# Performance work log

Hardware: AMD Instinct MI355X
Metric: run time of the kernel (lower is better)

The kernel has to match this reference:

```python
import jax, jax.numpy as jnp
import numpy as np

EMBEDDING_DIM = 256
NUM_EMBEDDINGS = 2048
COMMITMENT_COST = 0.25


def setup_inputs() -> dict:
    key = jax.random.key(0)
    k1, k2 = jax.random.split(key)
    inputs = jax.random.normal(k1, (32, EMBEDDING_DIM, 32, 32), dtype=jnp.float32)
    # learned codebook buffer, shape (D, K) as in the torch module
    embedding = jax.random.normal(k2, (EMBEDDING_DIM, NUM_EMBEDDINGS), dtype=jnp.float32)
    return {"inputs": inputs, "embedding": embedding}


def reference(inputs, embedding):
    # Eval-mode forward of VectorQuantizerEMA (EMA buffer updates are
    # training-only side effects and do not affect the returned values).
    B, D, H, W = inputs.shape
    K = embedding.shape[1]
    x = inputs.astype(jnp.float32)
    # (B, D, H, W) -> (N, D), N = B*H*W, clamped as in the source
    flat = jnp.clip(jnp.transpose(x, (0, 2, 3, 1)).reshape(-1, D), -10.0, 10.0)
    # squared L2 distances to every codeword: (N, K)
    distances = (
        jnp.sum(flat * flat, axis=1, keepdims=True)
        + jnp.sum(embedding * embedding, axis=0, keepdims=True)
        - 2.0 * (flat @ embedding)
    )
    encoding_indices = jnp.argmin(distances, axis=1)  # (N,)
    # one-hot @ emb.T is just a gather of codebook columns
    q_flat = jnp.take(embedding.T, encoding_indices, axis=0)  # (N, D)
    quantized = jnp.transpose(q_flat.reshape(B, H, W, D), (0, 3, 1, 2))
    # VQ losses (computed against the un-clamped float inputs, as in torch)
    e_latent_loss = jnp.mean((jax.lax.stop_gradient(quantized) - x) ** 2)
    q_latent_loss = jnp.mean((quantized - jax.lax.stop_gradient(x)) ** 2)
    loss = q_latent_loss + COMMITMENT_COST * e_latent_loss
    # straight-through estimator
    quantized_st = inputs + jax.lax.stop_gradient(quantized - inputs)
    # perplexity from codeword usage (mean one-hot == normalized counts)
    n = encoding_indices.shape[0]
    avg_probs = jnp.zeros((K,), dtype=jnp.float32).at[encoding_indices].add(1.0) / n
    perplexity = jnp.exp(-jnp.sum(avg_probs * jnp.log(avg_probs + 1e-10)))
    return quantized_st, loss, perplexity, encoding_indices
```

## Files before the change

kernel.cpp:

```cpp
#include <hip/hip_runtime.h>
#include <hip/hip_bf16.h>
#include <math.h>

typedef unsigned int  uint;
typedef unsigned short ushort;

#define DD    256
#define KK    2048
#define HW    1024
#define NN    32768
#define NUMEL 8388608
#define STRIDEB (DD*HW)

#define WS_H2     0
#define WS_COUNTS 8192
#define WS_EBF    16512
#define WS_PV     2113664
#define WS_PI     2375808

#define OUT_LOSS  8388608
#define OUT_PPL   8388609
#define OUT_IDX   8388610

typedef __attribute__((ext_vector_type(8))) short  short8;
typedef __attribute__((ext_vector_type(4))) float  float4v;

typedef __attribute__((address_space(1))) uint guint;
typedef __attribute__((address_space(3))) uint luint;

__device__ __forceinline__ ushort f2bf(float f) {
    uint u = __float_as_uint(f);
    return (ushort)((u + 0x7FFFu + ((u >> 16) & 1u)) >> 16);
}

__global__ __launch_bounds__(256) void prep_emb(const float* __restrict__ emb,
                                                ushort* __restrict__ ebf,
                                                float* __restrict__ h2) {
    int g  = blockIdx.x * 256 + threadIdx.x;
    int k  = g & (KK - 1);
    int dg = g >> 11;
    int d0 = dg * 8;
    int s    = dg >> 2;
    int quad = dg & 3;
    int ct   = k >> 4;
    int l    = quad * 16 + (k & 15);

    union { ushort us[8]; uint4 v; } hu, lu;
    float p2 = 0.f;
#pragma unroll
    for (int j = 0; j < 8; ++j) {
        float v = emb[(size_t)(d0 + j) * KK + k];
        p2 += v * v;
        ushort hb = f2bf(v);
        float  hf = __uint_as_float(((uint)hb) << 16);
        hu.us[j] = hb;
        lu.us[j] = f2bf(v - hf);
    }
    size_t hi_off = (size_t)(((ct * 8 + s) * 2 + 0) * 64 + l) * 8;
    size_t lo_off = (size_t)(((ct * 8 + s) * 2 + 1) * 64 + l) * 8;
    *(uint4*)(ebf + hi_off) = hu.v;
    *(uint4*)(ebf + lo_off) = lu.v;
    atomicAdd(&h2[k], 0.5f * p2);
}

__global__ __launch_bounds__(256, 2) void argmin_mfma(
    const float*  __restrict__ x,
    const ushort* __restrict__ ebf,
    const float*  __restrict__ h2,
    float* __restrict__ pv,
    int*   __restrict__ pi)
{
    __shared__ ushort sB[2][8192];
    __shared__ float  sH2[1024];

    const int tid  = threadIdx.x;
    const int w    = tid >> 6;
    const int lane = tid & 63;
    const int m    = lane & 15;
    const int quad = lane >> 4;

    const int rb = blockIdx.x >> 1;
    const int ch = blockIdx.x & 1;
    const int n0 = rb * 128 + w * 32;
    const int b  = n0 >> 10;
    const int hwb = n0 & 1023;
    const float* xb = x + (size_t)b * STRIDEB;
    const int cbase = ch * 1024;
    const int ctg0  = cbase >> 4;

    auto stage = [&](ushort* dst, int ctg) {
        const char* gs = (const char*)(ebf + (size_t)ctg * 8192) + tid * 16;
        char*       ls = (char*)dst + tid * 16;
#pragma unroll
        for (int i = 0; i < 4; ++i)
            __builtin_amdgcn_global_load_lds((guint*)(gs + i * 4096),
                                             (luint*)(ls + i * 4096),
                                             16, 0, 0);
    };

    stage(sB[0], ctg0);
    ((float4*)sH2)[tid] = ((const float4*)(h2 + cbase))[tid];

    short8 xh[2][8], xl[2][8];
    float xs2[2] = {0.f, 0.f};
#pragma unroll
    for (int st = 0; st < 2; ++st) {
        const int hw = hwb + st * 16 + m;
#pragma unroll
        for (int s = 0; s < 8; ++s) {
            const float* p = xb + (size_t)(s * 32 + quad * 8) * HW + hw;
            short8 hh, ll;
#pragma unroll
            for (int j = 0; j < 8; ++j) {
                float v = p[(size_t)j * HW];
                v = fminf(fmaxf(v, -10.f), 10.f);
                xs2[st] += v * v;
                ushort hb = f2bf(v);
                float  hf = __uint_as_float(((uint)hb) << 16);
                hh[j] = (short)hb;
                ll[j] = (short)f2bf(v - hf);
            }
            xh[st][s] = hh;
            xl[st][s] = ll;
        }
    }
#pragma unroll
    for (int st = 0; st < 2; ++st) {
        xs2[st] += __shfl_xor(xs2[st], 16, 64);
        xs2[st] += __shfl_xor(xs2[st], 32, 64);
    }

    float bv[2][4] = {{1e30f,1e30f,1e30f,1e30f},{1e30f,1e30f,1e30f,1e30f}};
    int   bi[2][4] = {{0,0,0,0},{0,0,0,0}};

    auto compute_tile = [&](const ushort* sbc, int ct) {
        float4v ahh0 = {0,0,0,0}, ahl0 = {0,0,0,0}, alh0 = {0,0,0,0};
        float4v ahh1 = {0,0,0,0}, ahl1 = {0,0,0,0}, alh1 = {0,0,0,0};
#pragma unroll
        for (int s = 0; s < 8; ++s) {
            short8 eh = *(const short8*)&sbc[(s * 2 + 0) * 512 + lane * 8];
            short8 el = *(const short8*)&sbc[(s * 2 + 1) * 512 + lane * 8];
            alh0 = __builtin_amdgcn_mfma_f32_16x16x32_bf16(xl[0][s], eh, alh0, 0, 0, 0);
            ahl0 = __builtin_amdgcn_mfma_f32_16x16x32_bf16(xh[0][s], el, ahl0, 0, 0, 0);
            ahh0 = __builtin_amdgcn_mfma_f32_16x16x32_bf16(xh[0][s], eh, ahh0, 0, 0, 0);
            alh1 = __builtin_amdgcn_mfma_f32_16x16x32_bf16(xl[1][s], eh, alh1, 0, 0, 0);
            ahl1 = __builtin_amdgcn_mfma_f32_16x16x32_bf16(xh[1][s], el, ahl1, 0, 0, 0);
            ahh1 = __builtin_amdgcn_mfma_f32_16x16x32_bf16(xh[1][s], eh, ahh1, 0, 0, 0);
        }
        const int c  = cbase + ct * 16 + m;
        const float hv = sH2[ct * 16 + m];
#pragma unroll
        for (int i = 0; i < 4; ++i) {
            float s0 = hv - (ahh0[i] + (ahl0[i] + alh0[i]));
            float s1 = hv - (ahh1[i] + (ahl1[i] + alh1[i]));
            if (s0 < bv[0][i]) { bv[0][i] = s0; bi[0][i] = c; }
            if (s1 < bv[1][i]) { bv[1][i] = s1; bi[1][i] = c; }
        }
    };

    __syncthreads();

    for (int ct = 0; ct < 64; ct += 2) {
        stage(sB[1], ctg0 + ct + 1);
        compute_tile(sB[0], ct);
        __syncthreads();
        stage(sB[0], (ct + 2 < 64) ? (ctg0 + ct + 2) : ctg0);
        compute_tile(sB[1], ct + 1);
        __syncthreads();
    }

#pragma unroll
    for (int st = 0; st < 2; ++st) {
#pragma unroll
        for (int i = 0; i < 4; ++i) {
            float v  = bv[st][i];
            int   ix = bi[st][i];
#pragma unroll
            for (int msk = 8; msk >= 1; msk >>= 1) {
                float ov = __shfl_xor(v, msk, 64);
                int   oi = __shfl_xor(ix, msk, 64);
                if (ov < v || (ov == v && oi < ix)) { v = ov; ix = oi; }
            }
            float xr = __shfl(xs2[st], quad * 4 + i, 16);
            if (m == 0) {
                int n = n0 + st * 16 + quad * 4 + i;
                pv[n * 2 + ch] = xr + 2.0f * v;
                pi[n * 2 + ch] = ix;
            }
        }
    }
}

__global__ __launch_bounds__(256) void quant_kernel(
    const float* __restrict__ emb,
    const float* __restrict__ pv,
    const int*   __restrict__ pi,
    float* __restrict__ out_idx_f,
    int*   __restrict__ counts,
    float* __restrict__ outq)
{
    __shared__ float sE[4096];
    __shared__ int   sIdx[1024];

    const int tid  = threadIdx.x;
    const int bidx = blockIdx.x;
    const int b    = bidx >> 7;
    const int dp   = bidx & 127;
    const int d0   = dp * 2;
    const int nbase = b * HW;

    {
        const float4* src = (const float4*)(emb + (size_t)d0 * KK);
        float4* dst = (float4*)sE;
#pragma unroll
        for (int i = 0; i < 4; ++i) dst[tid + i * 256] = src[tid + i * 256];
    }
    {
        const int n = nbase + tid * 4;
        const float4* pv4 = (const float4*)(pv + (size_t)n * 2);
        const int4*   pi4 = (const int4*)(pi + (size_t)n * 2);
        float4 pva = pv4[0], pvb = pv4[1];
        int4   pia = pi4[0], pib = pi4[1];
        int i0 = (pva.y < pva.x) ? pia.y : pia.x;
        int i1 = (pva.w < pva.z) ? pia.w : pia.z;
        int i2 = (pvb.y < pvb.x) ? pib.y : pib.x;
        int i3 = (pvb.w < pvb.z) ? pib.w : pib.z;
        i0 = min(max(i0, 0), KK - 1); i1 = min(max(i1, 0), KK - 1);
        i2 = min(max(i2, 0), KK - 1); i3 = min(max(i3, 0), KK - 1);
        sIdx[tid * 4 + 0] = i0; sIdx[tid * 4 + 1] = i1;
        sIdx[tid * 4 + 2] = i2; sIdx[tid * 4 + 3] = i3;
        if (d0 == 0) {
            float4 ixf = { (float)i0, (float)i1, (float)i2, (float)i3 };
            *(float4*)(out_idx_f + n) = ixf;
            atomicAdd(&counts[i0], 1);
            atomicAdd(&counts[i1], 1);
            atomicAdd(&counts[i2], 1);
            atomicAdd(&counts[i3], 1);
        }
    }
    __syncthreads();

    {
        const int e   = tid * 8;
        const int dl  = e >> 10;
        const int hw0 = e & 1023;
        const float* row = sE + dl * 2048;
        float q[8];
#pragma unroll
        for (int j = 0; j < 8; ++j) q[j] = row[sIdx[hw0 + j]];
        float4 q0 = { q[0], q[1], q[2], q[3] };
        float4 q1 = { q[4], q[5], q[6], q[7] };
        float* dst = outq + (size_t)bidx * 2048 + e;
        *(float4*)(dst + 0) = q0;
        *(float4*)(dst + 4) = q1;
    }
}

__global__ __launch_bounds__(1024) void finalize_kernel(
    const int* __restrict__ counts,
    const float* __restrict__ pv,
    float* __restrict__ out)
{
    __shared__ float redp[16], redl[16];
    int tid = threadIdx.x;
    float s = 0.f;
#pragma unroll
    for (int k = tid; k < KK; k += 1024) {
        float p = (float)counts[k] * (1.0f / (float)NN);
        s += p * logf(p + 1e-10f);
    }
    float ls = 0.f;
    for (int n = tid; n < NN; n += 1024) {
        float2 pp = *(const float2*)(pv + (size_t)n * 2);
        ls += fminf(pp.x, pp.y);
    }
#pragma unroll
    for (int off = 32; off > 0; off >>= 1) {
        s  += __shfl_down(s, off, 64);
        ls += __shfl_down(ls, off, 64);
    }
    if ((tid & 63) == 0) { redp[tid >> 6] = s; redl[tid >> 6] = ls; }
    __syncthreads();
    if (tid == 0) {
        float tot = 0.f, lsum = 0.f;
#pragma unroll
        for (int i = 0; i < 16; ++i) { tot += redp[i]; lsum += redl[i]; }
        out[OUT_PPL]  = expf(-tot);
        out[OUT_LOSS] = lsum * 1.25f / (float)NUMEL;
    }
}

extern "C" void kernel_launch(void* const* d_in, const int* in_sizes, int n_in,
                              void* d_out, int out_size, void* d_ws, size_t ws_size,
                              hipStream_t stream) {
    const float* x   = (const float*)d_in[0];
    const float* emb = (const float*)d_in[1];
    float* out = (float*)d_out;
    char*  ws  = (char*)d_ws;

    float*  h2     = (float*)(ws + WS_H2);
    int*    counts = (int*)(ws + WS_COUNTS);
    ushort* ebf    = (ushort*)(ws + WS_EBF);
    float*  pv     = (float*)(ws + WS_PV);
    int*    pi     = (int*)(ws + WS_PI);

    hipMemsetAsync(ws, 0, 16384, stream);
    prep_emb<<<256, 256, 0, stream>>>(emb, ebf, h2);
    argmin_mfma<<<512, 256, 0, stream>>>(x, ebf, h2, pv, pi);
    quant_kernel<<<4096, 256, 0, stream>>>(emb, pv, pi,
                                           out + OUT_IDX, counts, out);
    finalize_kernel<<<1, 1024, 0, stream>>>(counts, pv, out);
}
```

Before: 209.0 us.

## Fuse finalize into quant kernel, drop memset and atomics, compute loss directly

Removes the memset and the finalize kernel launch. Counts and the done flag are now zeroed in prep_emb, and the final perplexity and loss reduction runs in the last quant block, found via an atomic done counter. Per-codeword norm partials are written without atomics and summed in argmin, and the x-norm computation is dropped from argmin. Loss is instead recomputed from quant output minus x, which costs an extra read of x in quant_kernel. Indices are stored as ushort. Together these cut launch and sync overhead, at the cost of extra traffic and a last-block serialized reduction.

```diff
diff --git a/kernel.cpp b/kernel.cpp
--- a/kernel.cpp
+++ b/kernel.cpp
@@ -11,18 +11,22 @@
 #define NN    32768
 #define NUMEL 8388608
 #define STRIDEB (DD*HW)
-
-#define WS_H2     0
-#define WS_COUNTS 8192
-#define WS_EBF    16512
-#define WS_PV     2113664
-#define WS_PI     2375808
+#define NQBLK 4096
+
+#define WS_H2P    0
+#define WS_COUNTS 131072
+#define WS_DONE   139264
+#define WS_EBF    139392
+#define WS_PV     2236544
+#define WS_PI     2498688
+#define WS_BPART  WS_H2P
 
 #define OUT_LOSS  8388608
 #define OUT_PPL   8388609
 #define OUT_IDX   8388610
 
 typedef __attribute__((ext_vector_type(8))) short  short8;
+typedef __attribute__((ext_vector_type(8))) ushort ushort8;
 typedef __attribute__((ext_vector_type(4))) float  float4v;
 
 typedef __attribute__((address_space(1))) uint guint;
@@ -35,40 +39,49 @@
 
 __global__ __launch_bounds__(256) void prep_emb(const float* __restrict__ emb,
                                                 ushort* __restrict__ ebf,
-                                                float* __restrict__ h2) {
-    int g  = blockIdx.x * 256 + threadIdx.x;
-    int k  = g & (KK - 1);
-    int dg = g >> 11;
-    int d0 = dg * 8;
-    int s    = dg >> 2;
-    int quad = dg & 3;
-    int ct   = k >> 4;
-    int l    = quad * 16 + (k & 15);
-
-    union { ushort us[8]; uint4 v; } hu, lu;
+                                                float* __restrict__ h2p,
+                                                int* __restrict__ counts,
+                                                int* __restrict__ done) {
+    int g   = blockIdx.x * 256 + threadIdx.x;
+    int k   = g & (KK - 1);
+    int dg2 = g >> 11;
+    int ct  = k >> 4;
     float p2 = 0.f;
 #pragma unroll
-    for (int j = 0; j < 8; ++j) {
-        float v = emb[(size_t)(d0 + j) * KK + k];
-        p2 += v * v;
-        ushort hb = f2bf(v);
-        float  hf = __uint_as_float(((uint)hb) << 16);
-        hu.us[j] = hb;
-        lu.us[j] = f2bf(v - hf);
-    }
-    size_t hi_off = (size_t)(((ct * 8 + s) * 2 + 0) * 64 + l) * 8;
-    size_t lo_off = (size_t)(((ct * 8 + s) * 2 + 1) * 64 + l) * 8;
-    *(uint4*)(ebf + hi_off) = hu.v;
-    *(uint4*)(ebf + lo_off) = lu.v;
-    atomicAdd(&h2[k], 0.5f * p2);
+    for (int h = 0; h < 2; ++h) {
+        int dg = dg2 * 2 + h;
+        int d0 = dg * 8;
+        int s    = dg >> 2;
+        int quad = dg & 3;
+        int l    = quad * 16 + (k & 15);
+        union { ushort us[8]; uint4 v; } hu, lu;
+#pragma unroll
+        for (int j = 0; j < 8; ++j) {
+            float v = emb[(size_t)(d0 + j) * KK + k];
+            p2 += v * v;
+            ushort hb = f2bf(v);
+            float  hf = __uint_as_float(((uint)hb) << 16);
+            hu.us[j] = hb;
+            lu.us[j] = f2bf(v - hf);
+        }
+        size_t hi_off = (size_t)(((ct * 8 + s) * 2 + 0) * 64 + l) * 8;
+        size_t lo_off = (size_t)(((ct * 8 + s) * 2 + 1) * 64 + l) * 8;
+        *(uint4*)(ebf + hi_off) = hu.v;
+        *(uint4*)(ebf + lo_off) = lu.v;
+    }
+    h2p[dg2 * 2048 + k] = 0.5f * p2;
+    if (blockIdx.x == 0) {
+        for (int i = threadIdx.x; i < KK; i += 256) counts[i] = 0;
+        if (threadIdx.x == 0) *done = 0;
+    }
 }
 
 __global__ __launch_bounds__(256, 2) void argmin_mfma(
     const float*  __restrict__ x,
     const ushort* __restrict__ ebf,
-    const float*  __restrict__ h2,
-    float* __restrict__ pv,
-    int*   __restrict__ pi)
+    const float*  __restrict__ h2p,
+    float*  __restrict__ pv,
+    ushort* __restrict__ pi)
 {
     __shared__ ushort sB[2][8192];
     __shared__ float  sH2[1024];
@@ -99,10 +112,17 @@
     };
 
     stage(sB[0], ctg0);
-    ((float4*)sH2)[tid] = ((const float4*)(h2 + cbase))[tid];
+    {
+        float4 a = {0.f, 0.f, 0.f, 0.f};
+#pragma unroll
+        for (int d = 0; d < 16; ++d) {
+            float4 v = ((const float4*)(h2p + d * 2048 + cbase))[tid];
+            a.x += v.x; a.y += v.y; a.z += v.z; a.w += v.w;
+        }
+        ((float4*)sH2)[tid] = a;
+    }
 
     short8 xh[2][8], xl[2][8];
-    float xs2[2] = {0.f, 0.f};
 #pragma unroll
     for (int st = 0; st < 2; ++st) {
         const int hw = hwb + st * 16 + m;
@@ -114,7 +134,6 @@
             for (int j = 0; j < 8; ++j) {
                 float v = p[(size_t)j * HW];
                 v = fminf(fmaxf(v, -10.f), 10.f);
-                xs2[st] += v * v;
                 ushort hb = f2bf(v);
                 float  hf = __uint_as_float(((uint)hb) << 16);
                 hh[j] = (short)hb;
@@ -123,11 +142,6 @@
             xh[st][s] = hh;
             xl[st][s] = ll;
         }
-    }
-#pragma unroll
-    for (int st = 0; st < 2; ++st) {
-        xs2[st] += __shfl_xor(xs2[st], 16, 64);
-        xs2[st] += __shfl_xor(xs2[st], 32, 64);
     }
 
     float bv[2][4] = {{1e30f,1e30f,1e30f,1e30f},{1e30f,1e30f,1e30f,1e30f}};
@@ -181,26 +195,29 @@
                 int   oi = __shfl_xor(ix, msk, 64);
                 if (ov < v || (ov == v && oi < ix)) { v = ov; ix = oi; }
             }
-            float xr = __shfl(xs2[st], quad * 4 + i, 16);
             if (m == 0) {
                 int n = n0 + st * 16 + quad * 4 + i;
-                pv[n * 2 + ch] = xr + 2.0f * v;
-                pi[n * 2 + ch] = ix;
+                pv[n * 2 + ch] = v;
+                pi[n * 2 + ch] = (ushort)min(max(ix, 0), KK - 1);
             }
         }
     }
 }
 
 __global__ __launch_bounds__(256) void quant_kernel(
-    const float* __restrict__ emb,
-    const float* __restrict__ pv,
-    const int*   __restrict__ pi,
-    float* __restrict__ out_idx_f,
+    const float*  __restrict__ x,
+    const float*  __restrict__ emb,
+    const float*  __restrict__ pv,
+    const ushort* __restrict__ pi,
     int*   __restrict__ counts,
-    float* __restrict__ outq)
+    float* __restrict__ out,
+    float* __restrict__ bpart,
+    int*   __restrict__ done)
 {
     __shared__ float sE[4096];
     __shared__ int   sIdx[1024];
+    __shared__ float red[4], redl[4];
+    __shared__ int   sLast;
 
     const int tid  = threadIdx.x;
     const int bidx = blockIdx.x;
@@ -218,20 +235,19 @@
     {
         const int n = nbase + tid * 4;
         const float4* pv4 = (const float4*)(pv + (size_t)n * 2);
-        const int4*   pi4 = (const int4*)(pi + (size_t)n * 2);
         float4 pva = pv4[0], pvb = pv4[1];
-        int4   pia = pi4[0], pib = pi4[1];
-        int i0 = (pva.y < pva.x) ? pia.y : pia.x;
-        int i1 = (pva.w < pva.z) ? pia.w : pia.z;
-        int i2 = (pvb.y < pvb.x) ? pib.y : pib.x;
-        int i3 = (pvb.w < pvb.z) ? pib.w : pib.z;
-        i0 = min(max(i0, 0), KK - 1); i1 = min(max(i1, 0), KK - 1);
-        i2 = min(max(i2, 0), KK - 1); i3 = min(max(i3, 0), KK - 1);
+        ushort8 pp = *(const ushort8*)(pi + (size_t)n * 2);
+        int i0 = (pva.y < pva.x) ? (int)pp[1] : (int)pp[0];
+        int i1 = (pva.w < pva.z) ? (int)pp[3] : (int)pp[2];
+        int i2 = (pvb.y < pvb.x) ? (int)pp[5] : (int)pp[4];
+        int i3 = (pvb.w < pvb.z) ? (int)pp[7] : (int)pp[6];
+        i0 = min(i0, KK - 1); i1 = min(i1, KK - 1);
+        i2 = min(i2, KK - 1); i3 = min(i3, KK - 1);
         sIdx[tid * 4 + 0] = i0; sIdx[tid * 4 + 1] = i1;
         sIdx[tid * 4 + 2] = i2; sIdx[tid * 4 + 3] = i3;
         if (d0 == 0) {
             float4 ixf = { (float)i0, (float)i1, (float)i2, (float)i3 };
-            *(float4*)(out_idx_f + n) = ixf;
+            *(float4*)(out + OUT_IDX + n) = ixf;
             atomicAdd(&counts[i0], 1);
             atomicAdd(&counts[i1], 1);
             atomicAdd(&counts[i2], 1);
@@ -240,6 +256,7 @@
     }
     __syncthreads();
 
+    float s;
     {
         const int e   = tid * 8;
         const int dl  = e >> 10;
@@ -248,45 +265,49 @@
         float q[8];
 #pragma unroll
         for (int j = 0; j < 8; ++j) q[j] = row[sIdx[hw0 + j]];
+        const size_t go = (size_t)bidx * 2048 + e;
+        const float4 xv0 = *(const float4*)(x + go);
+        const float4 xv1 = *(const float4*)(x + go + 4);
         float4 q0 = { q[0], q[1], q[2], q[3] };
         float4 q1 = { q[4], q[5], q[6], q[7] };
-        float* dst = outq + (size_t)bidx * 2048 + e;
-        *(float4*)(dst + 0) = q0;
-        *(float4*)(dst + 4) = q1;
-    }
-}
-
-__global__ __launch_bounds__(1024) void finalize_kernel(
-    const int* __restrict__ counts,
-    const float* __restrict__ pv,
-    float* __restrict__ out)
-{
-    __shared__ float redp[16], redl[16];
-    int tid = threadIdx.x;
-    float s = 0.f;
-#pragma unroll
-    for (int k = tid; k < KK; k += 1024) {
-        float p = (float)counts[k] * (1.0f / (float)NN);
-        s += p * logf(p + 1e-10f);
-    }
-    float ls = 0.f;
-    for (int n = tid; n < NN; n += 1024) {
-        float2 pp = *(const float2*)(pv + (size_t)n * 2);
-        ls += fminf(pp.x, pp.y);
-    }
-#pragma unroll
-    for (int off = 32; off > 0; off >>= 1) {
-        s  += __shfl_down(s, off, 64);
-        ls += __shfl_down(ls, off, 64);
-    }
-    if ((tid & 63) == 0) { redp[tid >> 6] = s; redl[tid >> 6] = ls; }
-    __syncthreads();
-    if (tid == 0) {
-        float tot = 0.f, lsum = 0.f;
-#pragma unroll
-        for (int i = 0; i < 16; ++i) { tot += redp[i]; lsum += redl[i]; }
-        out[OUT_PPL]  = expf(-tot);
-        out[OUT_LOSS] = lsum * 1.25f / (float)NUMEL;
+        *(float4*)(out + go)     = q0;
+        *(float4*)(out + go + 4) = q1;
+        float a0 = q0.x - xv0.x, a1 = q0.y - xv0.y, a2 = q0.z - xv0.z, a3 = q0.w - xv0.w;
+        float a4 = q1.x - xv1.x, a5 = q1.y - xv1.y, a6 = q1.z - xv1.z, a7 = q1.w - xv1.w;
+        s = a0*a0 + a1*a1 + a2*a2 + a3*a3 + a4*a4 + a5*a5 + a6*a6 + a7*a7;
+    }
+#pragma unroll
+    for (int off = 32; off > 0; off >>= 1) s += __shfl_down(s, off, 64);
+    if ((tid & 63) == 0) red[tid >> 6] = s;
+    __syncthreads();
+    if (tid == 0) bpart[bidx] = red[0] + red[1] + red[2] + red[3];
+
+    __threadfence();
+    __syncthreads();
+    if (tid == 0) { int prev = atomicAdd(done, 1); sLast = (prev == NQBLK - 1); }
+    __syncthreads();
+    if (sLast) {
+        __threadfence();
+        float sp = 0.f;
+        for (int k = tid; k < KK; k += 256) {
+            float p = (float)counts[k] * (1.0f / (float)NN);
+            sp += p * logf(p + 1e-10f);
+        }
+        float ls = 0.f;
+        for (int i = tid; i < NQBLK; i += 256) ls += bpart[i];
+#pragma unroll
+        for (int off = 32; off > 0; off >>= 1) {
+            sp += __shfl_down(sp, off, 64);
+            ls += __shfl_down(ls, off, 64);
+        }
+        if ((tid & 63) == 0) { red[tid >> 6] = sp; redl[tid >> 6] = ls; }
+        __syncthreads();
+        if (tid == 0) {
+            float tot  = red[0] + red[1] + red[2] + red[3];
+            float lsum = redl[0] + redl[1] + redl[2] + redl[3];
+            out[OUT_PPL]  = expf(-tot);
+            out[OUT_LOSS] = lsum * 1.25f / (float)NUMEL;
+        }
     }
 }
 
@@ -298,16 +319,15 @@
     float* out = (float*)d_out;
     char*  ws  = (char*)d_ws;
 
-    float*  h2     = (float*)(ws + WS_H2);
+    float*  h2p    = (float*)(ws + WS_H2P);
     int*    counts = (int*)(ws + WS_COUNTS);
+    int*    done   = (int*)(ws + WS_DONE);
     ushort* ebf    = (ushort*)(ws + WS_EBF);
     float*  pv     = (float*)(ws + WS_PV);
-    int*    pi     = (int*)(ws + WS_PI);
-
-    hipMemsetAsync(ws, 0, 16384, stream);
-    prep_emb<<<256, 256, 0, stream>>>(emb, ebf, h2);
-    argmin_mfma<<<512, 256, 0, stream>>>(x, ebf, h2, pv, pi);
-    quant_kernel<<<4096, 256, 0, stream>>>(emb, pv, pi,
-                                           out + OUT_IDX, counts, out);
-    finalize_kernel<<<1, 1024, 0, stream>>>(counts, pv, out);
-}
+    ushort* pi     = (ushort*)(ws + WS_PI);
+    float*  bpart  = (float*)(ws + WS_BPART);
+
+    prep_emb<<<128, 256, 0, stream>>>(emb, ebf, h2p, counts, done);
+    argmin_mfma<<<512, 256, 0, stream>>>(x, ebf, h2p, pv, pi);
+    quant_kernel<<<NQBLK, 256, 0, stream>>>(x, emb, pv, pi, counts, out, bpart, done);
+}
```

After: 688.7 us. +229.5%, slower.
